# Performance work log

Measured on AMD Instinct MI355X. Metric: run time of the kernel, lower is better.

The kernel has to match this reference:

```python
import jax, jax.numpy as jnp
import numpy as np
from jax import lax

KERNEL = 3      # patch size
STRIDE = 1      # matching stride at low res
RATE = 2        # downsample rate
SOFTMAX_SCALE = 10.0


def _extract_patches(img, k, stride):
    """tf.image.extract_patches with SAME padding. img: [B,H,W,C] -> [B, oh*ow, k, k, C]."""
    B, H, W, C = img.shape
    oh = -(-H // stride)
    ow = -(-W // stride)
    ph = max((oh - 1) * stride + k - H, 0)
    pw = max((ow - 1) * stride + k - W, 0)
    img = jnp.pad(img, ((0, 0), (ph // 2, ph - ph // 2), (pw // 2, pw - pw // 2), (0, 0)))
    # stack the k*k shifted strided views; channel-last order matches TF's (kh, kw, C) flattening
    cols = [img[:, dh:dh + (oh - 1) * stride + 1:stride, dw:dw + (ow - 1) * stride + 1:stride, :]
            for dh in range(k) for dw in range(k)]
    p = jnp.stack(cols, axis=3)  # [B, oh, ow, k*k, C]
    return p.reshape(B, oh * ow, k, k, C)


def _avgpool2(x):
    """Exact equivalent of TF bilinear (antialias=False) downsample by factor 2."""
    B, H, W, C = x.shape
    return x.reshape(B, H // 2, 2, W // 2, 2, C).mean(axis=(2, 4))


def _conv_same(x4, w):
    return lax.conv_general_dilated(x4, w, (1, 1), 'SAME',
                                    dimension_numbers=('NHWC', 'HWIO', 'NHWC'))


def _forward(x, mask):
    B, H, W, C = x.shape
    k, stride, rate = KERNEL, STRIDE, RATE
    h, w = H // rate, W // rate
    L = h * w

    # raw (full-res) patches used for reconstruction: [B,k,k,C,L]
    raw_w = jnp.transpose(_extract_patches(x, k, rate * stride), (0, 2, 3, 4, 1))
    # low-res foreground / background (identical here, as in the source)
    f = _avgpool2(x)              # [B,h,w,C]
    m = _avgpool2(mask)           # [B,h,w,1]
    # low-res matching patches: [B,k,k,C,L]
    wp = jnp.transpose(_extract_patches(f, k, stride), (0, 2, 3, 4, 1))
    # mask patches -> gate: mm = 1 where the 3x3 mask patch mean is exactly 1.0
    mp = _extract_patches(m, k, stride)                       # [B,L,k,k,1]
    mm = (jnp.mean(mp, axis=(2, 3, 4)) == 1.0).astype(jnp.float32)  # [B,L]

    fuse_w = jnp.eye(KERNEL, dtype=jnp.float32).reshape(KERNEL, KERNEL, 1, 1)

    def per_item(xi, wi, rwi, mmi):
        # xi:[h,w,C]  wi,rwi:[k,k,C,L]  mmi:[L]
        wn = wi / jnp.maximum(jnp.sqrt(jnp.sum(wi * wi, axis=(0, 1, 2))), 1e-4)
        yi = _conv_same(xi[None], wn)          # [1,h,w,L] cosine-similarity logits
        att = yi[0]
        # fuse: diagonal conv over the [L,L] score matrix in both patch orderings
        z = yi.reshape(1, L, L, 1)
        z = _conv_same(z, fuse_w)
        z = z.reshape(1, h, w, h, w).transpose(0, 2, 1, 4, 3).reshape(1, L, L, 1)
        z = _conv_same(z, fuse_w)
        z = z.reshape(1, w, h, w, h).transpose(0, 2, 1, 4, 3)
        yi = z.reshape(1, h, w, L)
        mm4 = mmi.reshape(1, 1, 1, L)
        yi = jax.nn.softmax(yi * mm4 * SOFTMAX_SCALE, axis=3) * mm4
        # reconstruction: transposed conv with raw full-res patches as filters
        out = lax.conv_transpose(yi, rwi, (rate, rate), 'SAME',
                                 dimension_numbers=('NHWC', 'HWIO', 'NHWC'),
                                 transpose_kernel=True) / float(rate * rate)
        return out[0], att

    y, att = jax.vmap(per_item)(f, wp, raw_w, mm)
    return y, att


def setup_inputs() -> dict:
    key = jax.random.key(0)
    x = jax.random.normal(key, (2, 128, 128, 64), dtype=jnp.float32)
    # binary hole mask: ones inside a centered 64x64 square
    mask = jnp.zeros((2, 128, 128, 1), jnp.float32).at[:, 32:96, 32:96, :].set(1.0)
    return {"x": x, "mask": mask}


def reference(x, mask):
    return _forward(x, mask)
```

## Files before the change

### kernel.cpp

```cpp
#include <hip/hip_runtime.h>
#include <hip/hip_bf16.h>

typedef _Float16 f16x8 __attribute__((ext_vector_type(8)));
typedef float f32x4 __attribute__((ext_vector_type(4)));

__device__ __forceinline__ void gload_lds16(const void* gptr, void* lptr) {
  __builtin_amdgcn_global_load_lds(
      (const __attribute__((address_space(1))) void*)gptr,
      (__attribute__((address_space(3))) void*)lptr, 16, 0, 0);
}

__global__ void k_pre(const float* __restrict__ x, const float* __restrict__ mask,
                      _Float16* __restrict__ f_h, float* __restrict__ sumsq,
                      float* __restrict__ mlow) {
  int blk = blockIdx.x;
  int b = blk >> 12, ij = blk & 4095;
  int i = ij >> 6, j = ij & 63;
  int c = threadIdx.x;
  size_t base = ((size_t)(b * 128 + 2 * i) * 128 + 2 * j) * 64 + c;
  float f = 0.25f * (x[base] + x[base + 64] + x[base + 128 * 64] + x[base + 128 * 64 + 64]);
  f_h[(size_t)blk * 64 + c] = (_Float16)f;
  float fsq = f * f;
  for (int off = 32; off; off >>= 1) fsq += __shfl_down(fsq, off);
  if (c == 0) {
    sumsq[blk] = fsq;
    size_t mb = (size_t)(b * 128 + 2 * i) * 128 + 2 * j;
    mlow[blk] = 0.25f * (mask[mb] + mask[mb + 1] + mask[mb + 128] + mask[mb + 129]);
  }
}

__global__ void k_norm_mm(const float* __restrict__ sumsq, const float* __restrict__ mlow,
                          float* __restrict__ invn, float* __restrict__ mmb) {
  int t = blockIdx.x * 256 + threadIdx.x;
  int b = t >> 12, l = t & 4095;
  int li = l >> 6, lj = l & 63;
  float s = 0.f;
  bool ok = true;
  for (int dh = -1; dh <= 1; ++dh)
    for (int dw = -1; dw <= 1; ++dw) {
      int ii = li + dh, jj = lj + dw;
      float mv = 0.f;
      if ((unsigned)ii < 64u && (unsigned)jj < 64u) {
        int idx = (b << 12) + ii * 64 + jj;
        s += sumsq[idx];
        mv = mlow[idx];
      }
      ok = ok && (mv == 1.0f);
    }
  invn[t] = 1.0f / fmaxf(sqrtf(s), 1e-4f);
  mmb[t] = ok ? 1.0f : 0.0f;
}

__global__ void k_compact(const float* __restrict__ mmb, int* __restrict__ actIdx,
                          int* __restrict__ nAct) {
  int b = blockIdx.x;
  int t = threadIdx.x;
  __shared__ int sbuf[256];
  __shared__ int sbase;
  if (t == 0) sbase = 0;
  __syncthreads();
  for (int chunk = 0; chunk < 16; ++chunk) {
    int l = chunk * 256 + t;
    int flag = (mmb[(b << 12) + l] == 1.0f) ? 1 : 0;
    sbuf[t] = flag;
    __syncthreads();
    for (int off = 1; off < 256; off <<= 1) {
      int v = (t >= off) ? sbuf[t - off] : 0;
      __syncthreads();
      sbuf[t] += v;
      __syncthreads();
    }
    int incl = sbuf[t];
    int excl = incl - flag;
    int base = sbase;
    if (flag) {
      int pos = base + excl;
      if (pos < 1024) actIdx[(b << 10) + pos] = l;
    }
    __syncthreads();
    if (t == 255) sbase = base + incl;
    __syncthreads();
  }
  int total = sbase;
  for (int slot = t; slot < 1024; slot += 256)
    if (slot >= total) actIdx[(b << 10) + slot] = 0;
  if (t == 0) nAct[b] = (total > 1024) ? 1024 : total;
}

__global__ void k_build_p(const _Float16* __restrict__ f_h, _Float16* __restrict__ P) {
  int blk = blockIdx.x;
  int b = blk >> 12, l = blk & 4095;
  int li = l >> 6, lj = l & 63, c = threadIdx.x;
  _Float16* dst = P + (size_t)blk * 576 + c;
#pragma unroll
  for (int kk = 0; kk < 9; ++kk) {
    int kh = kk / 3, kw = kk % 3;
    int ii = li + kh - 1, jj = lj + kw - 1;
    _Float16 v = (_Float16)0.f;
    if ((unsigned)ii < 64u && (unsigned)jj < 64u)
      v = f_h[((size_t)(b << 12) + ii * 64 + jj) * 64 + c];
    dst[kk * 64] = v;
  }
}

__global__ void k_build_rt(const float* __restrict__ x, _Float16* __restrict__ Rt) {
  int kh = blockIdx.x, li = blockIdx.y, b = blockIdx.z;
  int r = 2 * li + kh;
  if (r >= 128) return;
  __shared__ float xrow[128 * 65];
  for (int t = threadIdx.x; t < 8192; t += 256) {
    int v = t >> 6, c = t & 63;
    xrow[v * 65 + c] = x[((size_t)(b * 128 + r) * 128 + v) * 64 + c];
  }
  __syncthreads();
  for (int idx = threadIdx.x; idx < 12288; idx += 256) {
    int lj = idx & 63, rest = idx >> 6;
    int c = rest & 63, kw = rest >> 6;
    int v = 2 * lj + kw;
    float val = (v < 128) ? xrow[v * 65 + c] : 0.f;
    int n = (kh * 3 + kw) * 64 + c;
    Rt[((size_t)b * 640 + n) * 4096 + li * 64 + lj] = (_Float16)val;
  }
}

__global__ void k_rtsub(const _Float16* __restrict__ Rt, const int* __restrict__ actIdx,
                        _Float16* __restrict__ Rts) {
  int n = blockIdx.x, b = blockIdx.y;
  const _Float16* src = Rt + ((size_t)b * 640 + n) * 4096;
  _Float16* dst = Rts + ((size_t)b * 640 + n) * 1024;
  const int* aIdx = actIdx + (b << 10);
  for (int s = threadIdx.x; s < 1024; s += 256) dst[s] = src[aIdx[s]];
}

__global__ __launch_bounds__(256) void k_gemm_sim(const _Float16* __restrict__ P,
                                                  const float* __restrict__ invn,
                                                  float* __restrict__ att) {
  int b = blockIdx.z;
  const _Float16* Ab = P + (size_t)b * 4096 * 576;
  int rowBase = blockIdx.y * 128, colBase = blockIdx.x * 128;
  __shared__ alignas(16) _Float16 As[128 * 32];
  __shared__ alignas(16) _Float16 Bs[128 * 32];
  int tid = threadIdx.x, wave = tid >> 6, lane = tid & 63;
  int q = lane >> 4, rr = lane & 15;
  int wr = (wave >> 1) * 64, wc = (wave & 1) * 64;
  f32x4 acc[4][4] = {};
  for (int kt = 0; kt < 576; kt += 32) {
    __syncthreads();
#pragma unroll
    for (int t = 0; t < 2; ++t) {
      int chunk = t * 256 + wave * 64 + lane;
      int row = chunk >> 2, kc = (chunk & 3) * 8;
      gload_lds16(Ab + (size_t)(rowBase + row) * 576 + kt + kc,
                  As + (size_t)(t * 256 + wave * 64) * 8);
      gload_lds16(Ab + (size_t)(colBase + row) * 576 + kt + kc,
                  Bs + (size_t)(t * 256 + wave * 64) * 8);
    }
    __syncthreads();
    f16x8 af[4], bf[4];
#pragma unroll
    for (int mi = 0; mi < 4; ++mi)
      af[mi] = *(const f16x8*)(As + (wr + mi * 16 + rr) * 32 + q * 8);
#pragma unroll
    for (int ni = 0; ni < 4; ++ni)
      bf[ni] = *(const f16x8*)(Bs + (wc + ni * 16 + rr) * 32 + q * 8);
#pragma unroll
    for (int mi = 0; mi < 4; ++mi)
#pragma unroll
      for (int ni = 0; ni < 4; ++ni)
        acc[mi][ni] = __builtin_amdgcn_mfma_f32_16x16x32_f16(af[mi], bf[ni], acc[mi][ni], 0, 0, 0);
  }
  float* attb = att + ((size_t)b << 24);
#pragma unroll
  for (int ni = 0; ni < 4; ++ni) {
    int gc = colBase + wc + ni * 16 + rr;
    float sc = invn[(b << 12) + gc];
#pragma unroll
    for (int mi = 0; mi < 4; ++mi)
#pragma unroll
      for (int reg = 0; reg < 4; ++reg) {
        int gr = rowBase + wr + mi * 16 + q * 4 + reg;
        attb[((size_t)gr << 12) + gc] = acc[mi][ni][reg] * sc;
      }
  }
}

__global__ __launch_bounds__(256) void k_fuse_softmax2(const float* __restrict__ att,
                                                       const int* __restrict__ actIdx,
                                                       const int* __restrict__ nAct,
                                                       _Float16* __restrict__ Asub) {
  int blk = blockIdx.x;
  int b = blk >> 12, p = blk & 4095;
  const float* Y = att + ((size_t)b << 24);
  const int* aIdx = actIdx + (b << 10);
  int na = nAct[b];
  int tid = threadIdx.x;
  int pi = p >> 6, pj = p & 63;
  int acol = pj * 64 + pi;
  float z[4];
  float mx = (na < 4096) ? 0.f : -1e30f;
#pragma unroll
  for (int s4 = 0; s4 < 4; ++s4) {
    int slot = s4 * 256 + tid;
    float zz = -1e30f;
    if (slot < na) {
      int l = aIdx[slot];
      int li = l >> 6, lj = l & 63;
      int bcol = lj * 64 + li;
      float F = 0.f;
#pragma unroll
      for (int d2 = -1; d2 <= 1; ++d2) {
        int a2 = acol + d2, b2 = bcol + d2;
        if ((unsigned)a2 < 4096u && (unsigned)b2 < 4096u) {
          int p2 = (a2 & 63) * 64 + (a2 >> 6);
          int l2 = (b2 & 63) * 64 + (b2 >> 6);
#pragma unroll
          for (int d1 = -1; d1 <= 1; ++d1) {
            int qq = p2 + d1, rr2 = l2 + d1;
            if ((unsigned)qq < 4096u && (unsigned)rr2 < 4096u)
              F += Y[((size_t)qq << 12) + rr2];
          }
        }
      }
      zz = F * 10.f;
    }
    z[s4] = zz;
    mx = fmaxf(mx, zz);
  }
  __shared__ float red[4];
  for (int off = 32; off; off >>= 1) mx = fmaxf(mx, __shfl_down(mx, off));
  if ((tid & 63) == 0) red[tid >> 6] = mx;
  __syncthreads();
  mx = fmaxf(fmaxf(red[0], red[1]), fmaxf(red[2], red[3]));
  float e[4];
  float esum = 0.f;
#pragma unroll
  for (int s4 = 0; s4 < 4; ++s4) {
    int slot = s4 * 256 + tid;
    e[s4] = (slot < na) ? __expf(z[s4] - mx) : 0.f;
    esum += e[s4];
  }
  for (int off = 32; off; off >>= 1) esum += __shfl_down(esum, off);
  __syncthreads();
  if ((tid & 63) == 0) red[tid >> 6] = esum;
  __syncthreads();
  float total = red[0] + red[1] + red[2] + red[3] + (float)(4096 - na) * __expf(0.f - mx);
  float inv = 1.f / total;
  _Float16* Ap = Asub + ((size_t)blk << 10);
#pragma unroll
  for (int s4 = 0; s4 < 4; ++s4) Ap[s4 * 256 + tid] = (_Float16)(e[s4] * inv);
}

__global__ __launch_bounds__(256) void k_gemm_recon(const _Float16* __restrict__ Asub,
                                                    const _Float16* __restrict__ Rts,
                                                    float* __restrict__ y) {
  int b = blockIdx.z;
  const _Float16* Ab = Asub + ((size_t)b << 22);
  const _Float16* Bb = Rts + (size_t)b * 640 * 1024;
  int rowBase = blockIdx.y * 128, colBase = blockIdx.x * 128;
  __shared__ alignas(16) _Float16 As[128 * 32];
  __shared__ alignas(16) _Float16 Bs[128 * 32];
  int tid = threadIdx.x, wave = tid >> 6, lane = tid & 63;
  int q = lane >> 4, rr = lane & 15;
  int wr = (wave >> 1) * 64, wc = (wave & 1) * 64;
  f32x4 acc[4][4] = {};
  for (int kt = 0; kt < 1024; kt += 32) {
    __syncthreads();
#pragma unroll
    for (int t = 0; t < 2; ++t) {
      int chunk = t * 256 + wave * 64 + lane;
      int row = chunk >> 2, kc = (chunk & 3) * 8;
      gload_lds16(Ab + ((size_t)(rowBase + row) << 10) + kt + kc,
                  As + (size_t)(t * 256 + wave * 64) * 8);
      gload_lds16(Bb + ((size_t)(colBase + row) << 10) + kt + kc,
                  Bs + (size_t)(t * 256 + wave * 64) * 8);
    }
    __syncthreads();
    f16x8 af[4], bf[4];
#pragma unroll
    for (int mi = 0; mi < 4; ++mi)
      af[mi] = *(const f16x8*)(As + (wr + mi * 16 + rr) * 32 + q * 8);
#pragma unroll
    for (int ni = 0; ni < 4; ++ni)
      bf[ni] = *(const f16x8*)(Bs + (wc + ni * 16 + rr) * 32 + q * 8);
#pragma unroll
    for (int mi = 0; mi < 4; ++mi)
#pragma unroll
      for (int ni = 0; ni < 4; ++ni)
        acc[mi][ni] = __builtin_amdgcn_mfma_f32_16x16x32_f16(af[mi], bf[ni], acc[mi][ni], 0, 0, 0);
  }
#pragma unroll
  for (int ni = 0; ni < 4; ++ni) {
    int gc = colBase + wc + ni * 16 + rr;
    if (gc < 576) {
      int kk = gc >> 6, c = gc & 63;
      int kh = kk / 3, kw = kk - kh * 3;
#pragma unroll
      for (int mi = 0; mi < 4; ++mi)
#pragma unroll
        for (int reg = 0; reg < 4; ++reg) {
          int gp = rowBase + wr + mi * 16 + q * 4 + reg;
          int i = gp >> 6, j = gp & 63;
          int u = 2 * i + kh, v = 2 * j + kw;
          if (u < 128 && v < 128)
            atomicAdd(y + (((size_t)((b * 128 + u) * 128 + v)) << 6) + c,
                      0.25f * acc[mi][ni][reg]);
        }
    }
  }
}

extern "C" void kernel_launch(void* const* d_in, const int* in_sizes, int n_in,
                              void* d_out, int out_size, void* d_ws, size_t ws_size,
                              hipStream_t stream) {
  const float* x = (const float*)d_in[0];
  const float* mask = (const float*)d_in[1];
  float* out = (float*)d_out;
  float* y = out;
  float* att = out + 2097152;

  char* ws = (char*)d_ws;
  _Float16* f_h = (_Float16*)(ws + 0);
  float* sumsq = (float*)(ws + 0x100000);
  float* mlow = (float*)(ws + 0x108000);
  float* invn = (float*)(ws + 0x110000);
  float* mmb = (float*)(ws + 0x118000);
  _Float16* P = (_Float16*)(ws + 0x120000);
  _Float16* Rt = (_Float16*)(ws + 0xA20000);
  int* actIdx = (int*)(ws + 0x1420000);
  int* nAct = (int*)(ws + 0x1422000);
  _Float16* Rts = (_Float16*)(ws + 0x1430000);
  _Float16* Asub = (_Float16*)(ws + 0x16B0000);
  (void)in_sizes; (void)n_in; (void)out_size; (void)ws_size;

  hipMemsetAsync(y, 0, (size_t)2097152 * 4, stream);
  hipMemsetAsync(Rt, 0, (size_t)2 * 640 * 4096 * 2, stream);

  k_pre<<<8192, 64, 0, stream>>>(x, mask, f_h, sumsq, mlow);
  k_norm_mm<<<32, 256, 0, stream>>>(sumsq, mlow, invn, mmb);
  k_compact<<<2, 256, 0, stream>>>(mmb, actIdx, nAct);
  k_build_p<<<8192, 64, 0, stream>>>(f_h, P);
  k_build_rt<<<dim3(3, 64, 2), 256, 0, stream>>>(x, Rt);
  k_rtsub<<<dim3(640, 2), 256, 0, stream>>>(Rt, actIdx, Rts);
  k_gemm_sim<<<dim3(32, 32, 2), 256, 0, stream>>>(P, invn, att);
  k_fuse_softmax2<<<8192, 256, 0, stream>>>(att, actIdx, nAct, Asub);
  k_gemm_recon<<<dim3(5, 32, 2), 256, 0, stream>>>(Asub, Rts, y);
}
```

Measured before the change: 324.6 us.

## Exploit Gram-matrix symmetry in similarity GEMM and use ballot-based compaction scan

The similarity GEMM P·P^T is symmetric, so only upper-triangular 128x128 tiles are computed (528 per batch instead of 1024). Each off-diagonal tile also writes its mirrored transpose through an LDS staging buffer, with the column norm scale applied. Diagonal tiles reuse the A tile for B and skip the second load. Separately, the compaction prefix sum now uses wave ballot/popcount instead of a barrier-heavy LDS scan. The trade-off is extra LDS for the transpose buffer, additional barriers and stores per tile, and fewer blocks in flight.

```diff
diff --git a/kernel.cpp b/kernel.cpp
--- a/kernel.cpp
+++ b/kernel.cpp
@@ -55,30 +55,26 @@
                           int* __restrict__ nAct) {
   int b = blockIdx.x;
   int t = threadIdx.x;
-  __shared__ int sbuf[256];
+  int lane = t & 63, wv = t >> 6;
+  __shared__ int wsum[4];
   __shared__ int sbase;
   if (t == 0) sbase = 0;
   __syncthreads();
   for (int chunk = 0; chunk < 16; ++chunk) {
     int l = chunk * 256 + t;
     int flag = (mmb[(b << 12) + l] == 1.0f) ? 1 : 0;
-    sbuf[t] = flag;
-    __syncthreads();
-    for (int off = 1; off < 256; off <<= 1) {
-      int v = (t >= off) ? sbuf[t - off] : 0;
-      __syncthreads();
-      sbuf[t] += v;
-      __syncthreads();
-    }
-    int incl = sbuf[t];
-    int excl = incl - flag;
-    int base = sbase;
+    unsigned long long m = __ballot(flag);
+    int wpre = __popcll(m & ((1ull << lane) - 1ull));
+    if (lane == 0) wsum[wv] = __popcll(m);
+    __syncthreads();
+    int off = sbase;
+    for (int w2 = 0; w2 < wv; ++w2) off += wsum[w2];
     if (flag) {
-      int pos = base + excl;
+      int pos = off + wpre;
       if (pos < 1024) actIdx[(b << 10) + pos] = l;
     }
     __syncthreads();
-    if (t == 255) sbase = base + incl;
+    if (t == 0) sbase += wsum[0] + wsum[1] + wsum[2] + wsum[3];
     __syncthreads();
   }
   int total = sbase;
@@ -137,9 +133,17 @@
                                                   float* __restrict__ att) {
   int b = blockIdx.z;
   const _Float16* Ab = P + (size_t)b * 4096 * 576;
-  int rowBase = blockIdx.y * 128, colBase = blockIdx.x * 128;
+  int idx = blockIdx.x;
+  int bj = (int)((sqrtf(8.f * (float)idx + 1.f) - 1.f) * 0.5f);
+  while ((bj + 1) * (bj + 2) / 2 <= idx) ++bj;
+  while (bj * (bj + 1) / 2 > idx) --bj;
+  int bi = idx - bj * (bj + 1) / 2;
+  int rowBase = bi * 128, colBase = bj * 128;
+  bool diag = (bi == bj);
+
   __shared__ alignas(16) _Float16 As[128 * 32];
   __shared__ alignas(16) _Float16 Bs[128 * 32];
+  __shared__ alignas(16) float tbuf[32][132];
   int tid = threadIdx.x, wave = tid >> 6, lane = tid & 63;
   int q = lane >> 4, rr = lane & 15;
   int wr = (wave >> 1) * 64, wc = (wave & 1) * 64;
@@ -152,17 +156,19 @@
       int row = chunk >> 2, kc = (chunk & 3) * 8;
       gload_lds16(Ab + (size_t)(rowBase + row) * 576 + kt + kc,
                   As + (size_t)(t * 256 + wave * 64) * 8);
-      gload_lds16(Ab + (size_t)(colBase + row) * 576 + kt + kc,
-                  Bs + (size_t)(t * 256 + wave * 64) * 8);
-    }
-    __syncthreads();
+      if (!diag)
+        gload_lds16(Ab + (size_t)(colBase + row) * 576 + kt + kc,
+                    Bs + (size_t)(t * 256 + wave * 64) * 8);
+    }
+    __syncthreads();
+    const _Float16* Bsrc = diag ? As : Bs;
     f16x8 af[4], bf[4];
 #pragma unroll
     for (int mi = 0; mi < 4; ++mi)
       af[mi] = *(const f16x8*)(As + (wr + mi * 16 + rr) * 32 + q * 8);
 #pragma unroll
     for (int ni = 0; ni < 4; ++ni)
-      bf[ni] = *(const f16x8*)(Bs + (wc + ni * 16 + rr) * 32 + q * 8);
+      bf[ni] = *(const f16x8*)(Bsrc + (wc + ni * 16 + rr) * 32 + q * 8);
 #pragma unroll
     for (int mi = 0; mi < 4; ++mi)
 #pragma unroll
@@ -181,6 +187,34 @@
         int gr = rowBase + wr + mi * 16 + q * 4 + reg;
         attb[((size_t)gr << 12) + gc] = acc[mi][ni][reg] * sc;
       }
+  }
+  if (diag) return;
+  const float* ivrow = invn + (b << 12) + rowBase;
+#pragma unroll
+  for (int ph = 0; ph < 4; ++ph) {
+    __syncthreads();
+    if ((ph >> 1) == (wc >> 6)) {
+      int nlo = (ph & 1) * 2;
+#pragma unroll
+      for (int nn = 0; nn < 2; ++nn) {
+        int ni = nlo + nn;
+        int rloc = nn * 16 + rr;
+#pragma unroll
+        for (int mi = 0; mi < 4; ++mi)
+          *(f32x4*)&tbuf[rloc][wr + mi * 16 + q * 4] = acc[mi][ni];
+      }
+    }
+    __syncthreads();
+    int r = tid >> 3;
+    int cbase = (tid & 7) * 16;
+    int grow = colBase + ph * 32 + r;
+    float* dst = attb + ((size_t)grow << 12) + rowBase + cbase;
+#pragma unroll
+    for (int cc = 0; cc < 16; cc += 4) {
+      f32x4 v = *(f32x4*)&tbuf[r][cbase + cc];
+      f32x4 s = *(const f32x4*)(ivrow + cbase + cc);
+      *(f32x4*)(dst + cc) = v * s;
+    }
   }
 }
 
@@ -341,7 +375,7 @@
   k_build_p<<<8192, 64, 0, stream>>>(f_h, P);
   k_build_rt<<<dim3(3, 64, 2), 256, 0, stream>>>(x, Rt);
   k_rtsub<<<dim3(640, 2), 256, 0, stream>>>(Rt, actIdx, Rts);
-  k_gemm_sim<<<dim3(32, 32, 2), 256, 0, stream>>>(P, invn, att);
+  k_gemm_sim<<<dim3(528, 1, 2), 256, 0, stream>>>(P, invn, att);
   k_fuse_softmax2<<<8192, 256, 0, stream>>>(att, actIdx, nAct, Asub);
   k_gemm_recon<<<dim3(5, 32, 2), 256, 0, stream>>>(Asub, Rts, y);
 }
```

Measured after the change: 321.3 us. No clear change (-1.0%).
